# Kernel optimization log

Hardware: AMD Instinct MI355X
Metric: run time of the kernel (lower is better)

The kernel has to match this reference:

```python
import jax, jax.numpy as jnp
import numpy as np

KH, KW = 3, 3
SH, SW = 1, 1
IC, OC = 32, 32
M = 4
P = M * M
ITERS = 3
LAM = 1.0
EPS = 1e-8


def _patches(t, kh, kw, sh, sw):
    # t: [B, H, W, ...] -> [B, Ho, Wo, kh, kw, ...] (im2col, matches torch unfold+permute)
    H, W = t.shape[1], t.shape[2]
    Ho = (H - kh) // sh + 1
    Wo = (W - kw) // sw + 1
    i = (jnp.arange(Ho) * sh)[:, None] + jnp.arange(kh)[None, :]  # [Ho,kh]
    j = (jnp.arange(Wo) * sw)[:, None] + jnp.arange(kw)[None, :]  # [Wo,kw]
    tp = t[:, i]            # [B,Ho,kh,W,...]
    tp = tp[:, :, :, j]     # [B,Ho,kh,Wo,kw,...]
    return jnp.moveaxis(tp, 2, 3)  # [B,Ho,Wo,kh,kw,...]


def setup_inputs() -> dict:
    key = jax.random.key(0)
    k1, k2, k3, k4, k5 = jax.random.split(key, 5)
    x = jax.random.normal(k1, (4, 14, 14, IC, M, M), dtype=jnp.float32)
    a = jax.random.uniform(k2, (4, 14, 14, IC), dtype=jnp.float32)
    W = jax.random.uniform(k3, (KH, KW, IC, OC, M, M), dtype=jnp.float32)   # torch.rand init
    beta_u = jax.random.uniform(k4, (1, OC, 1), dtype=jnp.float32)
    beta_a = jax.random.uniform(k5, (1, OC), dtype=jnp.float32)
    return {"x": x, "a": a, "W": W, "beta_u": beta_u, "beta_a": beta_a}


def reference(x, a, W, beta_u, beta_a):
    # im2col patches
    xp = _patches(x, KH, KW, SH, SW)          # [B,Ho,Wo,kh,kw,IC,M,M]
    ap = _patches(a, KH, KW, SH, SW)          # [B,Ho,Wo,kh,kw,IC]
    # pose-transform votes: per (kh,kw,inCap,outCap) 4x4 matmul
    V = jnp.einsum('bhwklcxy,klcoyz->bhwklcoxz', xp, W)
    B, Ho, Wo = V.shape[:3]
    N = KH * KW * IC
    V = V.reshape(B, Ho, Wo, N, OC, P)        # votes
    a_in = ap.reshape(B, Ho, Wo, N)
    bu = beta_u.reshape(OC, 1)
    ba = beta_a.reshape(OC)

    # EM routing (Hinton et al. 2018, fixed inverse temperature)
    R = jnp.full((B, Ho, Wo, N, OC), 1.0 / OC, dtype=V.dtype)
    for it in range(ITERS):
        Ra = R * a_in[..., None]                                  # [B,Ho,Wo,N,OC]
        Rs = Ra.sum(axis=3) + EPS                                 # [B,Ho,Wo,OC]
        mu = jnp.einsum('bhwno,bhwnop->bhwop', Ra, V) / Rs[..., None]
        d = V - mu[:, :, :, None]                                 # [B,Ho,Wo,N,OC,P]
        sig2 = jnp.einsum('bhwno,bhwnop->bhwop', Ra, d * d) / Rs[..., None] + EPS
        cost = (bu + 0.5 * jnp.log(sig2)) * Rs[..., None]         # [B,Ho,Wo,OC,P]
        a_out = jax.nn.sigmoid(LAM * (ba - cost.sum(-1)))         # [B,Ho,Wo,OC]
        if it < ITERS - 1:
            logp = -0.5 * jnp.sum(d * d / sig2[:, :, :, None] + jnp.log(sig2)[:, :, :, None], axis=-1)
            R = jax.nn.softmax(jnp.log(a_out + EPS)[:, :, :, None] + logp, axis=-1)

    pose = mu.reshape(B, Ho, Wo, OC, M, M)
    return pose, a_out
```

## Files before the change

kernel.cpp:

```cpp
#include <hip/hip_runtime.h>


#define EPSV 1e-8f

typedef float v2f __attribute__((ext_vector_type(2)));
typedef float v4f __attribute__((ext_vector_type(4)));

#define PK_ADD(d, a, b) asm("v_pk_add_f32 %0, %1, %2" : "=v"(d) : "v"(a), "v"(b))
#define PK_MUL(d, a, b) asm("v_pk_mul_f32 %0, %1, %2" : "=v"(d) : "v"(a), "v"(b))
#define PK_FMA_ACC(acc, a, b) \
  asm("v_pk_fma_f32 %0, %1, %2, %0" : "+v"(acc) : "v"(a), "v"(b))
#define PK_MUL_BLO(d, a, b) \
  asm("v_pk_mul_f32 %0, %1, %2 op_sel:[0,0] op_sel_hi:[0,1]" : "=v"(d) : "v"(a), "v"(b))
#define PK_FMA_BLO_ACC(acc, a, b) \
  asm("v_pk_fma_f32 %0, %1, %2, %0 op_sel:[0,0,0] op_sel_hi:[0,1,1]" : "+v"(acc) : "v"(a), "v"(b))
#define PK_FMA_BHI_ACC(acc, a, b) \
  asm("v_pk_fma_f32 %0, %1, %2, %0 op_sel:[1,0,0] op_sel_hi:[1,1,1]" : "+v"(acc) : "v"(a), "v"(b))

template <int CTRL>
__device__ __forceinline__ float dppf(float v) {
  return __int_as_float(__builtin_amdgcn_update_dpp(
      0, __float_as_int(v), CTRL, 0xf, 0xf, true));
}
__device__ __forceinline__ float swz16(float v) {
  return __int_as_float(__builtin_amdgcn_ds_swizzle(__float_as_int(v), 0x401F));
}
__device__ __forceinline__ float red_max32(float v) {
  v = fmaxf(v, dppf<0xB1>(v));
  v = fmaxf(v, dppf<0x4E>(v));
  v = fmaxf(v, dppf<0x141>(v));
  v = fmaxf(v, dppf<0x140>(v));
  v = fmaxf(v, swz16(v));
  return v;
}
__device__ __forceinline__ float red_sum32(float v) {
  v += dppf<0xB1>(v);
  v += dppf<0x4E>(v);
  v += dppf<0x141>(v);
  v += dppf<0x140>(v);
  v += swz16(v);
  return v;
}

__device__ __forceinline__ void compute_votes_pk(const float* __restrict__ Wt,
                                                 const float* __restrict__ xr,
                                                 int n, int o, v2f* __restrict__ V2)
{
  v2f Wf2[8];
  {
    const float* wp = Wt + (((n << 5) + o) << 4);
#pragma unroll
    for (int i = 0; i < 4; ++i) {
      const v4f q = *(const v4f*)(wp + (i << 2));
      Wf2[i*2+0] = __builtin_shufflevector(q, q, 0, 1);
      Wf2[i*2+1] = __builtin_shufflevector(q, q, 2, 3);
    }
  }
  v2f xv2[8];
#pragma unroll
  for (int i = 0; i < 4; ++i) {
    const v4f q = *(const v4f*)(xr + (i << 2));
    xv2[i*2+0] = __builtin_shufflevector(q, q, 0, 1);
    xv2[i*2+1] = __builtin_shufflevector(q, q, 2, 3);
  }
#pragma unroll
  for (int xi = 0; xi < 4; ++xi) {
#pragma unroll
    for (int zp = 0; zp < 2; ++zp) {
      v2f acc;
      PK_MUL_BLO(acc, xv2[xi*2+0], Wf2[0*2+zp]);
      PK_FMA_BHI_ACC(acc, xv2[xi*2+0], Wf2[1*2+zp]);
      PK_FMA_BLO_ACC(acc, xv2[xi*2+1], Wf2[2*2+zp]);
      PK_FMA_BHI_ACC(acc, xv2[xi*2+1], Wf2[3*2+zp]);
      V2[xi*2+zp] = acc;
    }
  }
}

__global__ __launch_bounds__(512, 2) void caps_stats(
    const float* __restrict__ X, const float* __restrict__ A, const float* __restrict__ Wt,
    const float* __restrict__ Bu, const float* __restrict__ Ba,
    const float* __restrict__ prev, float* __restrict__ cur, int it)
{
  __shared__ float xp_s[144*16];
  __shared__ float a_s[144];
  __shared__ float part[8*544];
  __shared__ float prs[8*32];
  __shared__ float mu_t[512], isig_t[512], lsig_t[512];
  __shared__ float la_s[32], slog_s[32], rs_s[32];

  const int t    = threadIdx.x;
  const int o    = t & 31;
  const int ng   = t >> 5;
  const int wv   = t >> 6;
  const int lane = t & 63;

  const int bid  = blockIdx.x;
  const int pos  = bid >> 1;
  const int half = bid & 1;
  const int b  = pos / 144;
  const int r_ = pos - b*144;
  const int h  = r_ / 12;
  const int w  = r_ - (r_/12)*12;
  const int nbase = half * 144;

  for (int i = t; i < 576; i += 512) {
    const int r  = i >> 2, q4 = i & 3;
    const int n  = nbase + r;
    const int kl = n >> 5, c = n & 31;
    const int hy = h + kl/3, wx = w + (kl - (kl/3)*3);
    const float4 v = *(const float4*)(X + ((((b*14+hy)*14+wx) << 9) + (c << 4) + (q4 << 2)));
    *(float4*)(xp_s + (r << 4) + (q4 << 2)) = v;
  }
  if (t < 144) {
    const int n  = nbase + t;
    const int kl = n >> 5, c = n & 31;
    const int hy = h + kl/3, wx = w + (kl - (kl/3)*3);
    a_s[t] = A[((b*14+hy)*14+wx)*32 + c];
  }

  v2f mmu2[8], isig2[8];
  float la_r = 0.f, slog_r = 0.f;

  if (it > 0) {
    {
      const int pi = t >> 5, oo = t & 31;
      const float* h0 = prev + (pos*2+0)*1056;
      const float* h1 = prev + (pos*2+1)*1056;
      const int idx = pi*32 + oo;
      const float s1   = h0[idx]       + h1[idx];
      const float s2   = h0[512+idx]   + h1[512+idx];
      const float rsum = h0[1024+oo]   + h1[1024+oo] + EPSV;
      const float mu = s1 / rsum;
      float var = s2 / rsum - mu*mu;
      var = fmaxf(var, 0.f);
      const float sg = var + EPSV;
      mu_t[idx]   = mu;
      isig_t[idx] = 1.0f / sg;
      lsig_t[idx] = __logf(sg);
      if (pi == 0) rs_s[oo] = rsum;
    }
    __syncthreads();
    if (t < 32) {
      float slog = 0.f;
#pragma unroll
      for (int p = 0; p < 16; ++p) slog += lsig_t[p*32 + t];
      const float cost = rs_s[t] * (16.0f*Bu[t] + 0.5f*slog);
      const float av = 1.0f / (1.0f + __expf(-(Ba[t] - cost)));
      la_s[t]   = __logf(av + EPSV);
      slog_s[t] = slog;
    }
    __syncthreads();
#pragma unroll
    for (int pp = 0; pp < 8; ++pp) {
      mmu2[pp]  = (v2f){ -mu_t[(2*pp)*32 + o],  -mu_t[(2*pp+1)*32 + o] };
      isig2[pp] = (v2f){ isig_t[(2*pp)*32 + o], isig_t[(2*pp+1)*32 + o] };
    }
    slog_r = slog_s[o];
    la_r   = la_s[o];
  } else {
#pragma unroll
    for (int pp = 0; pp < 8; ++pp) { mmu2[pp] = (v2f)0.f; isig2[pp] = (v2f)0.f; }
    __syncthreads();
  }

  v2f S1_2[8], S2_2[8];
#pragma unroll
  for (int pp = 0; pp < 8; ++pp) { S1_2[pp] = (v2f)0.f; S2_2[pp] = (v2f)0.f; }
  float rs = 0.f;

#pragma unroll 1
  for (int j = 0; j < 9; ++j) {
    const int nl = ng + (j << 4);
    const int n  = nbase + nl;
    v2f V2[8];
    compute_votes_pk(Wt, xp_s + (nl << 4), n, o, V2);

    float ra;
    if (it == 0) {
      ra = a_s[nl] * (1.0f/32.0f);
    } else {
      v2f q2[4];
#pragma unroll
      for (int pp = 0; pp < 8; ++pp) {
        v2f d2, dd;
        PK_ADD(d2, V2[pp], mmu2[pp]);
        PK_MUL(dd, d2, d2);
        if (pp < 4) { PK_MUL(q2[pp], dd, isig2[pp]); }
        else        { PK_FMA_ACC(q2[pp-4], dd, isig2[pp]); }
      }
      v2f qa, qb;
      PK_ADD(qa, q2[0], q2[1]);
      PK_ADD(qb, q2[2], q2[3]);
      PK_ADD(qa, qa, qb);
      const float q = slog_r + (qa.x + qa.y);
      const float z = la_r - 0.5f*q;
      const float m  = red_max32(z);
      const float ev = __expf(z - m);
      const float s  = red_sum32(ev);
      ra = (ev / s) * a_s[nl];
    }
    rs += ra;
    {
      v2f raP = { ra, ra };
#pragma unroll
      for (int pp = 0; pp < 8; ++pp) {
        PK_FMA_ACC(S1_2[pp], raP, V2[pp]);
        v2f vv;
        PK_MUL(vv, V2[pp], V2[pp]);
        PK_FMA_ACC(S2_2[pp], raP, vv);
      }
    }
  }

  float S1[16], S2[16];
#pragma unroll
  for (int pp = 0; pp < 8; ++pp) {
    S1[2*pp] = S1_2[pp].x; S1[2*pp+1] = S1_2[pp].y;
    S2[2*pp] = S2_2[pp].x; S2[2*pp+1] = S2_2[pp].y;
  }
#pragma unroll
  for (int p = 0; p < 16; ++p) {
    S1[p] += __shfl_xor(S1[p], 32);
    S2[p] += __shfl_xor(S2[p], 32);
  }
  rs += __shfl_xor(rs, 32);

  float* dst = cur + bid*1056;

  if (lane < 32) {
    float* p1 = part + wv*544 + o*17;
#pragma unroll
    for (int p = 0; p < 16; ++p) p1[p] = S1[p];
    prs[wv*32 + o] = rs;
  }
  __syncthreads();
  {
    const int pi = t >> 5, oo = t & 31;
    float s1 = 0.f;
#pragma unroll
    for (int g = 0; g < 8; ++g) s1 += part[g*544 + oo*17 + pi];
    dst[t] = s1;
    if (t < 32) {
      float r = 0.f;
#pragma unroll
      for (int g = 0; g < 8; ++g) r += prs[(g << 5) + t];
      dst[1024 + t] = r;
    }
  }
  __syncthreads();

  if (lane < 32) {
    float* p2 = part + wv*544 + o*17;
#pragma unroll
    for (int p = 0; p < 16; ++p) p2[p] = S2[p];
  }
  __syncthreads();
  {
    const int pi = t >> 5, oo = t & 31;
    float s2 = 0.f;
#pragma unroll
    for (int g = 0; g < 8; ++g) s2 += part[g*544 + oo*17 + pi];
    dst[512 + t] = s2;
  }
}

__global__ __launch_bounds__(512, 4) void caps_final(
    const float* __restrict__ prev, const float* __restrict__ Bu,
    const float* __restrict__ Ba, float* __restrict__ Out)
{
  __shared__ float mu_t[512], lsig_t[512], rs_s[32], aout_s[32];

  const int t   = threadIdx.x;
  const int pos = blockIdx.x;
  {
    const int pi = t >> 5, oo = t & 31;
    const float* h0 = prev + (pos*2+0)*1056;
    const float* h1 = prev + (pos*2+1)*1056;
    const int idx = pi*32 + oo;
    const float s1   = h0[idx]     + h1[idx];
    const float s2   = h0[512+idx] + h1[512+idx];
    const float rsum = h0[1024+oo] + h1[1024+oo] + EPSV;
    const float mu = s1 / rsum;
    float var = s2 / rsum - mu*mu;
    var = fmaxf(var, 0.f);
    mu_t[idx]   = mu;
    lsig_t[idx] = __logf(var + EPSV);
    if (pi == 0) rs_s[oo] = rsum;
  }
  __syncthreads();
  if (t < 32) {
    float slog = 0.f;
#pragma unroll
    for (int p = 0; p < 16; ++p) slog += lsig_t[p*32 + t];
    const float cost = rs_s[t] * (16.0f*Bu[t] + 0.5f*slog);
    aout_s[t] = 1.0f / (1.0f + __expf(-(Ba[t] - cost)));
  }
  __syncthreads();
  {
    const int oo = t >> 4, pi = t & 15;
    Out[pos*512 + t] = mu_t[pi*32 + oo];
  }
  if (t < 32) Out[294912 + pos*32 + t] = aout_s[t];
}

extern "C" void kernel_launch(void* const* d_in, const int* in_sizes, int n_in,
                              void* d_out, int out_size, void* d_ws, size_t ws_size,
                              hipStream_t stream) {
  (void)in_sizes; (void)n_in; (void)ws_size; (void)out_size;
  const float* X  = (const float*)d_in[0];
  const float* A  = (const float*)d_in[1];
  const float* Wt = (const float*)d_in[2];
  const float* Bu = (const float*)d_in[3];
  const float* Ba = (const float*)d_in[4];
  float* Out = (float*)d_out;

  float* pa = (float*)d_ws;
  float* pb = pa + 1152*1056;

  hipLaunchKernelGGL(caps_stats, dim3(1152), dim3(512), 0, stream,
                     X, A, Wt, Bu, Ba, (const float*)nullptr, pa, 0);
  hipLaunchKernelGGL(caps_stats, dim3(1152), dim3(512), 0, stream,
                     X, A, Wt, Bu, Ba, pa, pb, 1);
  hipLaunchKernelGGL(caps_stats, dim3(1152), dim3(512), 0, stream,
                     X, A, Wt, Bu, Ba, pb, pa, 2);
  hipLaunchKernelGGL(caps_final, dim3(576), dim3(512), 0, stream,
                     pa, Bu, Ba, Out);
}
```

Before: 159.4 us.

## Process both input halves per block, halving grid and partial merges

Each caps_stats block now covers the full 288-input neighbourhood of one output position instead of half. Each thread computes two vote sets per loop iteration, interleaved, so the two independent softmax chains can overlap. This removes the two-half partial split and its merge reads, and it fetches each patch into shared memory once. In exchange the grid shrinks from 1152 to 576 blocks on a 256-CU device, and register and LDS pressure rise, which may lower occupancy below the launch-bounds target.

```diff
diff --git a/kernel.cpp b/kernel.cpp
--- a/kernel.cpp
+++ b/kernel.cpp
@@ -82,8 +82,8 @@
     const float* __restrict__ Bu, const float* __restrict__ Ba,
     const float* __restrict__ prev, float* __restrict__ cur, int it)
 {
-  __shared__ float xp_s[144*16];
-  __shared__ float a_s[144];
+  __shared__ float xp_s[288*16];
+  __shared__ float a_s[288];
   __shared__ float part[8*544];
   __shared__ float prs[8*32];
   __shared__ float mu_t[512], isig_t[512], lsig_t[512];
@@ -95,26 +95,21 @@
   const int wv   = t >> 6;
   const int lane = t & 63;
 
-  const int bid  = blockIdx.x;
-  const int pos  = bid >> 1;
-  const int half = bid & 1;
+  const int pos = blockIdx.x;
   const int b  = pos / 144;
   const int r_ = pos - b*144;
   const int h  = r_ / 12;
   const int w  = r_ - (r_/12)*12;
-  const int nbase = half * 144;
-
-  for (int i = t; i < 576; i += 512) {
+
+  for (int i = t; i < 1152; i += 512) {
     const int r  = i >> 2, q4 = i & 3;
-    const int n  = nbase + r;
-    const int kl = n >> 5, c = n & 31;
+    const int kl = r >> 5, c = r & 31;
     const int hy = h + kl/3, wx = w + (kl - (kl/3)*3);
     const float4 v = *(const float4*)(X + ((((b*14+hy)*14+wx) << 9) + (c << 4) + (q4 << 2)));
     *(float4*)(xp_s + (r << 4) + (q4 << 2)) = v;
   }
-  if (t < 144) {
-    const int n  = nbase + t;
-    const int kl = n >> 5, c = n & 31;
+  if (t < 288) {
+    const int kl = t >> 5, c = t & 31;
     const int hy = h + kl/3, wx = w + (kl - (kl/3)*3);
     a_s[t] = A[((b*14+hy)*14+wx)*32 + c];
   }
@@ -125,12 +120,11 @@
   if (it > 0) {
     {
       const int pi = t >> 5, oo = t & 31;
-      const float* h0 = prev + (pos*2+0)*1056;
-      const float* h1 = prev + (pos*2+1)*1056;
+      const float* hp = prev + (size_t)pos * 1056;
       const int idx = pi*32 + oo;
-      const float s1   = h0[idx]       + h1[idx];
-      const float s2   = h0[512+idx]   + h1[512+idx];
-      const float rsum = h0[1024+oo]   + h1[1024+oo] + EPSV;
+      const float s1   = hp[idx];
+      const float s2   = hp[512+idx];
+      const float rsum = hp[1024+oo] + EPSV;
       const float mu = s1 / rsum;
       float var = s2 / rsum - mu*mu;
       var = fmaxf(var, 0.f);
@@ -172,43 +166,54 @@
 #pragma unroll 1
   for (int j = 0; j < 9; ++j) {
     const int nl = ng + (j << 4);
-    const int n  = nbase + nl;
-    v2f V2[8];
-    compute_votes_pk(Wt, xp_s + (nl << 4), n, o, V2);
-
-    float ra;
+    v2f VA[8], VB[8];
+    compute_votes_pk(Wt, xp_s + (nl << 4),         nl,       o, VA);
+    compute_votes_pk(Wt, xp_s + ((nl + 144) << 4), nl + 144, o, VB);
+
+    float raA, raB;
     if (it == 0) {
-      ra = a_s[nl] * (1.0f/32.0f);
+      raA = a_s[nl]       * (1.0f/32.0f);
+      raB = a_s[nl + 144] * (1.0f/32.0f);
     } else {
-      v2f q2[4];
+      v2f qA2[4], qB2[4];
 #pragma unroll
       for (int pp = 0; pp < 8; ++pp) {
         v2f d2, dd;
-        PK_ADD(d2, V2[pp], mmu2[pp]);
-        PK_MUL(dd, d2, d2);
-        if (pp < 4) { PK_MUL(q2[pp], dd, isig2[pp]); }
-        else        { PK_FMA_ACC(q2[pp-4], dd, isig2[pp]); }
+        PK_ADD(d2, VA[pp], mmu2[pp]);  PK_MUL(dd, d2, d2);
+        if (pp < 4) { PK_MUL(qA2[pp], dd, isig2[pp]); }
+        else        { PK_FMA_ACC(qA2[pp-4], dd, isig2[pp]); }
+        PK_ADD(d2, VB[pp], mmu2[pp]);  PK_MUL(dd, d2, d2);
+        if (pp < 4) { PK_MUL(qB2[pp], dd, isig2[pp]); }
+        else        { PK_FMA_ACC(qB2[pp-4], dd, isig2[pp]); }
       }
       v2f qa, qb;
-      PK_ADD(qa, q2[0], q2[1]);
-      PK_ADD(qb, q2[2], q2[3]);
-      PK_ADD(qa, qa, qb);
-      const float q = slog_r + (qa.x + qa.y);
-      const float z = la_r - 0.5f*q;
-      const float m  = red_max32(z);
-      const float ev = __expf(z - m);
-      const float s  = red_sum32(ev);
-      ra = (ev / s) * a_s[nl];
-    }
-    rs += ra;
+      PK_ADD(qa, qA2[0], qA2[1]);  PK_ADD(qb, qA2[2], qA2[3]);  PK_ADD(qa, qa, qb);
+      const float qA = slog_r + (qa.x + qa.y);
+      PK_ADD(qa, qB2[0], qB2[1]);  PK_ADD(qb, qB2[2], qB2[3]);  PK_ADD(qa, qa, qb);
+      const float qB = slog_r + (qa.x + qa.y);
+      const float zA = la_r - 0.5f*qA;
+      const float zB = la_r - 0.5f*qB;
+      const float mA  = red_max32(zA);
+      const float mB  = red_max32(zB);
+      const float evA = __expf(zA - mA);
+      const float evB = __expf(zB - mB);
+      const float sA  = red_sum32(evA);
+      const float sB  = red_sum32(evB);
+      raA = (evA / sA) * a_s[nl];
+      raB = (evB / sB) * a_s[nl + 144];
+    }
+    rs += raA + raB;
     {
-      v2f raP = { ra, ra };
+      v2f rA = { raA, raA }, rB = { raB, raB };
 #pragma unroll
       for (int pp = 0; pp < 8; ++pp) {
-        PK_FMA_ACC(S1_2[pp], raP, V2[pp]);
+        PK_FMA_ACC(S1_2[pp], rA, VA[pp]);
         v2f vv;
-        PK_MUL(vv, V2[pp], V2[pp]);
-        PK_FMA_ACC(S2_2[pp], raP, vv);
+        PK_MUL(vv, VA[pp], VA[pp]);
+        PK_FMA_ACC(S2_2[pp], rA, vv);
+        PK_FMA_ACC(S1_2[pp], rB, VB[pp]);
+        PK_MUL(vv, VB[pp], VB[pp]);
+        PK_FMA_ACC(S2_2[pp], rB, vv);
       }
     }
   }
@@ -226,7 +231,7 @@
   }
   rs += __shfl_xor(rs, 32);
 
-  float* dst = cur + bid*1056;
+  float* dst = cur + (size_t)pos * 1056;
 
   if (lane < 32) {
     float* p1 = part + wv*544 + o*17;
@@ -275,12 +280,11 @@
   const int pos = blockIdx.x;
   {
     const int pi = t >> 5, oo = t & 31;
-    const float* h0 = prev + (pos*2+0)*1056;
-    const float* h1 = prev + (pos*2+1)*1056;
+    const float* hp = prev + (size_t)pos * 1056;
     const int idx = pi*32 + oo;
-    const float s1   = h0[idx]     + h1[idx];
-    const float s2   = h0[512+idx] + h1[512+idx];
-    const float rsum = h0[1024+oo] + h1[1024+oo] + EPSV;
+    const float s1   = hp[idx];
+    const float s2   = hp[512+idx];
+    const float rsum = hp[1024+oo] + EPSV;
     const float mu = s1 / rsum;
     float var = s2 / rsum - mu*mu;
     var = fmaxf(var, 0.f);
@@ -316,13 +320,13 @@
   float* Out = (float*)d_out;
 
   float* pa = (float*)d_ws;
-  float* pb = pa + 1152*1056;
-
-  hipLaunchKernelGGL(caps_stats, dim3(1152), dim3(512), 0, stream,
+  float* pb = pa + 576*1056;
+
+  hipLaunchKernelGGL(caps_stats, dim3(576), dim3(512), 0, stream,
                      X, A, Wt, Bu, Ba, (const float*)nullptr, pa, 0);
-  hipLaunchKernelGGL(caps_stats, dim3(1152), dim3(512), 0, stream,
+  hipLaunchKernelGGL(caps_stats, dim3(576), dim3(512), 0, stream,
                      X, A, Wt, Bu, Ba, pa, pb, 1);
-  hipLaunchKernelGGL(caps_stats, dim3(1152), dim3(512), 0, stream,
+  hipLaunchKernelGGL(caps_stats, dim3(576), dim3(512), 0, stream,
                      X, A, Wt, Bu, Ba, pb, pa, 2);
   hipLaunchKernelGGL(caps_final, dim3(576), dim3(512), 0, stream,
                      pa, Bu, Ba, Out);
```

After: 185.6 us. +16.4%, slower.
